# Kernel optimization log

Hardware: AMD Instinct MI355X
Metric: run time of the kernel (lower is better)

Reference implementation:

```python
import jax, jax.numpy as jnp
import numpy as np

G = 20000          # num_genes
B = 256            # batch_size
NNZ = 640000       # sparse adjacency nonzeros (avg degree 32)
K = 2              # PPR iterations
ALPHA = 0.1
NUM_CLASS = 33


def _spmm(rows, cols, vals, x):
    # y = A @ x with A sparse COO [G, G], x dense [G, B]
    return jax.ops.segment_sum(vals[:, None] * x[cols], rows, num_segments=G)


def setup_inputs() -> dict:
    key = jax.random.key(0)
    ks = jax.random.split(key, 18)
    inp = {
        "x_sample": jax.random.normal(ks[0], (B * G,), jnp.float32),
        "x_TF": jax.random.normal(ks[1], (B * G,), jnp.float32),
        "adj_rows": jax.random.randint(ks[2], (NNZ,), 0, G, jnp.int32),
        "adj_cols": jax.random.randint(ks[3], (NNZ,), 0, G, jnp.int32),
        "adj_vals": jax.random.uniform(ks[4], (NNZ,), jnp.float32) / 32.0,
        "adjT_rows": jax.random.randint(ks[5], (NNZ,), 0, G, jnp.int32),
        "adjT_cols": jax.random.randint(ks[6], (NNZ,), 0, G, jnp.int32),
        "adjT_vals": jax.random.uniform(ks[7], (NNZ,), jnp.float32) / 32.0,
        # learned scalar affine params (torch.rand(1))
        "emb_mut": jax.random.uniform(ks[8], (1,), jnp.float32),
        "bias_mut": jax.random.uniform(ks[9], (1,), jnp.float32),
        "emb_exp": jax.random.uniform(ks[10], (1,), jnp.float32),
        "bias_exp": jax.random.uniform(ks[11], (1,), jnp.float32),
        # MLP params (torch Linear layout: W [out, in])
        "W1": jax.random.normal(ks[12], (1024, G), jnp.float32) * (1.0 / np.sqrt(G)),
        "b1": jnp.zeros((1024,), jnp.float32),
        "W2": jax.random.normal(ks[13], (128, 1024), jnp.float32) * (1.0 / 32.0),
        "b2": jnp.zeros((128,), jnp.float32),
        "W3": jax.random.normal(ks[14], (NUM_CLASS, 128), jnp.float32) * (1.0 / np.sqrt(128.0)),
        "b3": jnp.zeros((NUM_CLASS,), jnp.float32),
    }
    return inp


def reference(x_sample, x_TF, adj_rows, adj_cols, adj_vals,
              adjT_rows, adjT_cols, adjT_vals,
              emb_mut, bias_mut, emb_exp, bias_exp,
              W1, b1, W2, b2, W3, b3):
    # scalar affine embedding + relu
    emb_m = jax.nn.relu(emb_mut * x_sample + bias_mut)   # [B*G]
    emb_e = jax.nn.relu(emb_exp * x_TF + bias_exp)       # [B*G]
    xs = emb_m.reshape(B, G).T                            # [G, B]
    xt = emb_e.reshape(B, G).T                            # [G, B]
    hs, ht = xs, xt
    one_m_a = 1.0 - ALPHA
    for _ in range(K):
        xs = _spmm(adj_rows, adj_cols, adj_vals, one_m_a * xs)
        xt = _spmm(adjT_rows, adjT_cols, adjT_vals, one_m_a * xt)
    xs = xs + ALPHA * hs
    xt = xt + ALPHA * ht
    hadamard = (xs * xt).T                                # [B, G]
    h1 = jax.nn.relu(hadamard @ W1.T + b1)                # [B, 1024]
    h2 = jax.nn.relu(h1 @ W2.T + b2)                      # [B, 128]
    return h2 @ W3.T + b3                                 # [B, num_class]
```

## Files before the change

### kernel.cpp

```cpp
#include <hip/hip_runtime.h>
#include <hip/hip_fp16.h>

#define G_   20000
#define B_   256
#define NNZ_ 640000
#define KCH_ 640
#define NZ_  32
#define NBUK 157
#define BCAP 4608
#define EPB  4000

typedef float f4 __attribute__((ext_vector_type(4)));
typedef _Float16 h8 __attribute__((ext_vector_type(8)));

__global__ __launch_bounds__(256) void zero_kernel(unsigned int* p, int n) {
    int i = blockIdx.x * 256 + threadIdx.x;
    if (i < n) p[i] = 0u;
}

__global__ __launch_bounds__(256) void embed_kernel(
        const float* __restrict__ xsamp, const float* __restrict__ xtf,
        const float* __restrict__ em, const float* __restrict__ bm,
        const float* __restrict__ ee, const float* __restrict__ be,
        __half* __restrict__ X0s, __half* __restrict__ X0t) {
    __shared__ float lds[64][65];
    const int t  = threadIdx.x;
    const int gb = blockIdx.x * 64, bb = blockIdx.y * 64;
    const float a_m = em[0], c_m = bm[0], a_e = ee[0], c_e = be[0];
    const int gl = t & 63, brow0 = t >> 6;
    const int cl = t & 31, row0  = t >> 5;
    const int g_l = gb + gl;
#pragma unroll
    for (int r = 0; r < 16; r++) {
        int bl = brow0 + r * 4;
        float v = 0.f;
        if (g_l < G_) v = xsamp[(size_t)(bb + bl) * G_ + g_l];
        lds[bl][gl] = fmaxf(a_m * v + c_m, 0.f);
    }
    __syncthreads();
#pragma unroll
    for (int r = 0; r < 8; r++) {
        int gl2 = row0 + r * 8;
        int g = gb + gl2;
        if (g < G_) {
            __half2 hv = __floats2half2_rn(lds[cl * 2][gl2], lds[cl * 2 + 1][gl2]);
            *(__half2*)(X0s + (size_t)g * B_ + bb + cl * 2) = hv;
        }
    }
    __syncthreads();
#pragma unroll
    for (int r = 0; r < 16; r++) {
        int bl = brow0 + r * 4;
        float v = 0.f;
        if (g_l < G_) v = xtf[(size_t)(bb + bl) * G_ + g_l];
        lds[bl][gl] = fmaxf(a_e * v + c_e, 0.f);
    }
    __syncthreads();
#pragma unroll
    for (int r = 0; r < 8; r++) {
        int gl2 = row0 + r * 8;
        int g = gb + gl2;
        if (g < G_) {
            __half2 hv = __floats2half2_rn(lds[cl * 2][gl2], lds[cl * 2 + 1][gl2]);
            *(__half2*)(X0t + (size_t)g * B_ + bb + cl * 2) = hv;
        }
    }
}

__global__ __launch_bounds__(256) void binsort_kernel(
        const int* __restrict__ rA, const int* __restrict__ cA, const float* __restrict__ vA,
        const int* __restrict__ rB, const int* __restrict__ cB, const float* __restrict__ vB,
        int2* __restrict__ metaA, int* __restrict__ cntA,
        int2* __restrict__ metaB, int* __restrict__ cntB) {
    __shared__ int2 stage[EPB];
    __shared__ unsigned char bkid[EPB];
    __shared__ int hist[NBUK], lstart[NBUK], gbase[NBUK];
    const int t = threadIdx.x;
    const int base = blockIdx.x * EPB;
    const int* rows; const int* colsp; const float* valsp; int2* meta; int* cnt;
    if (blockIdx.y == 0) { rows = rA; colsp = cA; valsp = vA; meta = metaA; cnt = cntA; }
    else                 { rows = rB; colsp = cB; valsp = vB; meta = metaB; cnt = cntB; }

    for (int i = t; i < NBUK; i += 256) hist[i] = 0;
    __syncthreads();
    for (int i = t; i < EPB; i += 256)
        atomicAdd(&hist[rows[base + i] >> 7], 1);
    __syncthreads();
    if (t == 0) {
        int s = 0;
        for (int b = 0; b < NBUK; b++) { lstart[b] = s; s += hist[b]; }
    }
    __syncthreads();
    if (t < NBUK) hist[t] = lstart[t];
    __syncthreads();
    for (int i = t; i < EPB; i += 256) {
        int r = rows[base + i];
        int c = colsp[base + i];
        float v = valsp[base + i];
        int b = r >> 7;
        int p = atomicAdd(&hist[b], 1);
        stage[p] = make_int2(((r & 127) << 24) | (c * (B_ * 2)),
                             __float_as_int(0.9f * v));
        bkid[p] = (unsigned char)b;
    }
    __syncthreads();
    if (t < NBUK) gbase[t] = atomicAdd(&cnt[t], hist[t] - lstart[t]);
    __syncthreads();
    for (int i = t; i < EPB; i += 256) {
        int b = bkid[i];
        meta[(size_t)b * BCAP + gbase[b] + (i - lstart[b])] = stage[i];
    }
}

__global__ __launch_bounds__(256) void rowsort_kernel(
        const int2* __restrict__ metaA, const int* __restrict__ cntA,
        int2* __restrict__ sortedA, int* __restrict__ rpA,
        const int2* __restrict__ metaB, const int* __restrict__ cntB,
        int2* __restrict__ sortedB, int* __restrict__ rpB) {
    __shared__ int2 stage[BCAP];
    __shared__ int2 sorted[BCAP];
    __shared__ int hist[2048];
    __shared__ int scanbuf[256];
    __shared__ int rowstart[128];
    __shared__ int carr[NBUK];
    const int t = threadIdx.x;
    const int buk = blockIdx.x;
    const int2* meta; const int* cnt; int2* outp; int* rp;
    if (blockIdx.y == 0) { meta = metaA; cnt = cntA; outp = sortedA; rp = rpA; }
    else                 { meta = metaB; cnt = cntB; outp = sortedB; rp = rpB; }

    if (t < NBUK) carr[t] = cnt[t];
    for (int i = t; i < 2048; i += 256) hist[i] = 0;
    __syncthreads();
    int bukStart = 0;
    const int nE = carr[buk];
    for (int b = 0; b < buk; b++) bukStart += carr[b];

    const int2* mp = meta + (size_t)buk * BCAP;
    for (int i = t; i < nE; i += 256) {
        int2 m = mp[i];
        stage[i] = m;
        unsigned ux = (unsigned)m.x;
        int key = ((ux >> 24) << 4) | ((ux & 0xFFFFFF) >> 20);
        atomicAdd(&hist[key], 1);
    }
    __syncthreads();
    int loc[8];
    {
        int s = 0;
#pragma unroll
        for (int i = 0; i < 8; i++) { loc[i] = s; s += hist[t * 8 + i]; }
        scanbuf[t] = s;
    }
    __syncthreads();
    for (int off = 1; off < 256; off <<= 1) {
        int v = scanbuf[t];
        int add = (t >= off) ? scanbuf[t - off] : 0;
        __syncthreads();
        scanbuf[t] = v + add;
        __syncthreads();
    }
    {
        int pre = (t == 0) ? 0 : scanbuf[t - 1];
#pragma unroll
        for (int i = 0; i < 8; i++) hist[t * 8 + i] = pre + loc[i];
    }
    __syncthreads();
    if (t < 128) rowstart[t] = hist[t << 4];
    __syncthreads();
    for (int i = t; i < nE; i += 256) {
        int2 m = stage[i];
        unsigned ux = (unsigned)m.x;
        int key = ((ux >> 24) << 4) | ((ux & 0xFFFFFF) >> 20);
        int p = atomicAdd(&hist[key], 1);
        sorted[p] = make_int2(m.x & 0xFFFFFF, m.y);
    }
    __syncthreads();
    for (int i = t; i < nE; i += 256)
        outp[bukStart + i] = sorted[i];
    if (t < 128) {
        int g = buk * 128 + t;
        if (g < G_) rp[g] = bukStart + rowstart[t];
    }
    if (buk == NBUK - 1 && t == 0) rp[G_] = bukStart + nE;
}

__global__ __launch_bounds__(256) void spmm_kernel(
        const int* __restrict__ rpA, const int2* __restrict__ metaA,
        const __half* __restrict__ xinA, __half* __restrict__ xoutA,
        const int* __restrict__ rpB, const int2* __restrict__ metaB,
        const __half* __restrict__ xinB, __half* __restrict__ xoutB) {
    const int bid   = blockIdx.x;
    const int combo = bid & 1;
    const int t = threadIdx.x;
    const int wave = t >> 6, lane = t & 63;
    const int g = (bid >> 1) * 4 + wave;
    const int* rp; const int2* meta; const __half* xin; __half* xout;
    if (combo == 0) { rp = rpA; meta = metaA; xin = xinA; xout = xoutA; }
    else            { rp = rpB; meta = metaB; xin = xinB; xout = xoutB; }
    const int beg = rp[g];
    const int n   = rp[g + 1] - beg;
    const char* xb = (const char*)xin + lane * 8;
    float a0 = 0.f, a1 = 0.f, a2 = 0.f, a3 = 0.f;
    int e = 0;
    for (; e + 4 <= n; e += 4) {
        int2 m0 = meta[beg + e],     m1 = meta[beg + e + 1];
        int2 m2 = meta[beg + e + 2], m3 = meta[beg + e + 3];
        float v0 = __int_as_float(m0.y);
        float v1 = __int_as_float(m1.y);
        float v2 = __int_as_float(m2.y);
        float v3 = __int_as_float(m3.y);
        uint2 r0 = *(const uint2*)(xb + m0.x);
        uint2 r1 = *(const uint2*)(xb + m1.x);
        uint2 r2 = *(const uint2*)(xb + m2.x);
        uint2 r3 = *(const uint2*)(xb + m3.x);
        float2 l0 = __half22float2(*(__half2*)&r0.x), h0 = __half22float2(*(__half2*)&r0.y);
        float2 l1 = __half22float2(*(__half2*)&r1.x), h1 = __half22float2(*(__half2*)&r1.y);
        float2 l2 = __half22float2(*(__half2*)&r2.x), h2 = __half22float2(*(__half2*)&r2.y);
        float2 l3 = __half22float2(*(__half2*)&r3.x), h3 = __half22float2(*(__half2*)&r3.y);
        a0 = fmaf(v0, l0.x, a0); a1 = fmaf(v0, l0.y, a1);
        a2 = fmaf(v0, h0.x, a2); a3 = fmaf(v0, h0.y, a3);
        a0 = fmaf(v1, l1.x, a0); a1 = fmaf(v1, l1.y, a1);
        a2 = fmaf(v1, h1.x, a2); a3 = fmaf(v1, h1.y, a3);
        a0 = fmaf(v2, l2.x, a0); a1 = fmaf(v2, l2.y, a1);
        a2 = fmaf(v2, h2.x, a2); a3 = fmaf(v2, h2.y, a3);
        a0 = fmaf(v3, l3.x, a0); a1 = fmaf(v3, l3.y, a1);
        a2 = fmaf(v3, h3.x, a2); a3 = fmaf(v3, h3.y, a3);
    }
    for (; e < n; ++e) {
        int2 m = meta[beg + e];
        float v = __int_as_float(m.y);
        uint2 r = *(const uint2*)(xb + m.x);
        float2 l = __half22float2(*(__half2*)&r.x), h = __half22float2(*(__half2*)&r.y);
        a0 = fmaf(v, l.x, a0); a1 = fmaf(v, l.y, a1);
        a2 = fmaf(v, h.x, a2); a3 = fmaf(v, h.y, a3);
    }
    __half2 o0 = __floats2half2_rn(a0, a1);
    __half2 o1 = __floats2half2_rn(a2, a3);
    uint2 ov;
    ov.x = *(unsigned*)&o0;
    ov.y = *(unsigned*)&o1;
    *(uint2*)((char*)xout + (size_t)g * (B_ * 2) + lane * 8) = ov;
}

__global__ __launch_bounds__(256) void combine_kernel(
        const __half* __restrict__ X2s, const __half* __restrict__ X0s,
        const __half* __restrict__ X2t, const __half* __restrict__ X0t,
        __half* __restrict__ hadBK) {
    __shared__ float lds[64][65];
    const int t = threadIdx.x;
    const int gb = blockIdx.x * 64, bb = blockIdx.y * 64;
    const int cl = t & 31, row0 = t >> 5;
#pragma unroll
    for (int r = 0; r < 8; r++) {
        int gl = row0 + r * 8;
        int g = gb + gl;
        float px = 0.f, py = 0.f;
        if (g < G_) {
            size_t idx = (size_t)g * B_ + bb + cl * 2;
            float2 x2s = __half22float2(*(const __half2*)(X2s + idx));
            float2 x0s = __half22float2(*(const __half2*)(X0s + idx));
            float2 x2t = __half22float2(*(const __half2*)(X2t + idx));
            float2 x0t = __half22float2(*(const __half2*)(X0t + idx));
            px = (x2s.x + 0.1f * x0s.x) * (x2t.x + 0.1f * x0t.x);
            py = (x2s.y + 0.1f * x0s.y) * (x2t.y + 0.1f * x0t.y);
        }
        lds[gl][cl * 2]     = px;
        lds[gl][cl * 2 + 1] = py;
    }
    __syncthreads();
#pragma unroll
    for (int r = 0; r < 8; r++) {
        int bl = row0 + r * 8;
        int g0 = gb + cl * 2;
        if (g0 < G_) {
            __half2 hv = __floats2half2_rn(lds[cl * 2][bl], lds[cl * 2 + 1][bl]);
            *(__half2*)(hadBK + (size_t)(bb + bl) * G_ + g0) = hv;
        }
    }
}

__global__ __launch_bounds__(512) void gemm1_kernel(
        const __half* __restrict__ hadBK, const float* __restrict__ W1,
        float* __restrict__ part) {
    __shared__ _Float16 a_lds[256][40];
    __shared__ _Float16 b_lds[128][40];
    const int t = threadIdx.x;
    const int lane = t & 63, wid = t >> 6;
    const int wm = wid >> 1, wn = wid & 1;
    const int l15 = lane & 15, l4 = lane >> 4;
    const int ob = blockIdx.x * 128;
    const int kb = blockIdx.y * KCH_;
    int kend = kb + KCH_; if (kend > G_) kend = G_;
    const int nsteps = (kend - kb) >> 5;
    const int ar = t >> 1, ah = t & 1;
    const int br = t >> 2, bs = t & 3;
    const _Float16* hadH = (const _Float16*)hadBK;
    const _Float16* asrc = hadH + (size_t)ar * G_ + ah * 16;
    const float*    bsrc = W1 + (size_t)(ob + br) * G_ + bs * 8;
    f4 acc[4][4] = {};
    h8 ra0 = *(const h8*)(asrc + kb);
    h8 ra1 = *(const h8*)(asrc + kb + 8);
    f4 rb0 = *(const f4*)(bsrc + kb);
    f4 rb1 = *(const f4*)(bsrc + kb + 4);
    for (int s = 0; s < nsteps; ++s) {
        *(h8*)&a_lds[ar][ah * 16]     = ra0;
        *(h8*)&a_lds[ar][ah * 16 + 8] = ra1;
        {
            h8 h;
            h[0] = (_Float16)rb0[0]; h[1] = (_Float16)rb0[1];
            h[2] = (_Float16)rb0[2]; h[3] = (_Float16)rb0[3];
            h[4] = (_Float16)rb1[0]; h[5] = (_Float16)rb1[1];
            h[6] = (_Float16)rb1[2]; h[7] = (_Float16)rb1[3];
            *(h8*)&b_lds[br][bs * 8] = h;
        }
        __syncthreads();
        if (s + 1 < nsteps) {
            const int k1 = kb + (s + 1) * 32;
            ra0 = *(const h8*)(asrc + k1);
            ra1 = *(const h8*)(asrc + k1 + 8);
            rb0 = *(const f4*)(bsrc + k1);
            rb1 = *(const f4*)(bsrc + k1 + 4);
        }
        h8 af[4], bf[4];
#pragma unroll
        for (int m = 0; m < 4; m++)
            af[m] = *(const h8*)&a_lds[wm * 64 + m * 16 + l15][l4 * 8];
#pragma unroll
        for (int n = 0; n < 4; n++)
            bf[n] = *(const h8*)&b_lds[wn * 64 + n * 16 + l15][l4 * 8];
#pragma unroll
        for (int m = 0; m < 4; m++)
#pragma unroll
            for (int n = 0; n < 4; n++)
                acc[m][n] = __builtin_amdgcn_mfma_f32_16x16x32_f16(
                    af[m], bf[n], acc[m][n], 0, 0, 0);
        __syncthreads();
    }
    const size_t zoff = (size_t)blockIdx.y * (B_ * 1024);
#pragma unroll
    for (int m = 0; m < 4; m++)
#pragma unroll
        for (int n = 0; n < 4; n++)
#pragma unroll
            for (int j = 0; j < 4; j++) {
                int b = wm * 64 + m * 16 + l4 * 4 + j;
                int o = ob + wn * 64 + n * 16 + l15;
                part[zoff + (size_t)b * 1024 + o] = acc[m][n][j];
            }
}

__global__ __launch_bounds__(256) void reduce_kernel(
        const float* __restrict__ part, const float* __restrict__ b1,
        float* __restrict__ h1) {
    int i = blockIdx.x * 256 + threadIdx.x;
    float s = 0.f;
#pragma unroll
    for (int z = 0; z < NZ_; z++) s += part[(size_t)z * 262144 + i];
    h1[i] = fmaxf(s + b1[i & 1023], 0.f);
}

__global__ __launch_bounds__(128) void gemm23_kernel(
        const float* __restrict__ h1, const float* __restrict__ W2,
        const float* __restrict__ b2, const float* __restrict__ W3,
        const float* __restrict__ b3, float* __restrict__ out) {
    __shared__ float h1row[1024];
    __shared__ float h2[128];
    const int b = blockIdx.x, t = threadIdx.x;
    *(f4*)&h1row[t * 4]       = *(const f4*)(h1 + (size_t)b * 1024 + t * 4);
    *(f4*)&h1row[512 + t * 4] = *(const f4*)(h1 + (size_t)b * 1024 + 512 + t * 4);
    __syncthreads();
    {
        float acc = b2[t];
        const f4* w  = (const f4*)(W2 + (size_t)t * 1024);
        const f4* hr = (const f4*)h1row;
        for (int k = 0; k < 256; k++) {
            f4 wv = w[k], hv = hr[k];
            acc += wv[0] * hv[0] + wv[1] * hv[1] + wv[2] * hv[2] + wv[3] * hv[3];
        }
        h2[t] = fmaxf(acc, 0.f);
    }
    __syncthreads();
    if (t < 33) {
        float acc = b3[t];
        const f4* w  = (const f4*)(W3 + (size_t)t * 128);
        const f4* hv = (const f4*)h2;
#pragma unroll
        for (int k = 0; k < 32; k++) {
            f4 a = w[k], x = hv[k];
            acc += a[0] * x[0] + a[1] * x[1] + a[2] * x[2] + a[3] * x[3];
        }
        out[b * 33 + t] = acc;
    }
}

extern "C" void kernel_launch(void* const* d_in, const int* in_sizes, int n_in,
                              void* d_out, int out_size, void* d_ws, size_t ws_size,
                              hipStream_t stream) {
    const float* x_sample  = (const float*)d_in[0];
    const float* x_TF      = (const float*)d_in[1];
    const int*   adj_rows  = (const int*)d_in[2];
    const int*   adj_cols  = (const int*)d_in[3];
    const float* adj_vals  = (const float*)d_in[4];
    const int*   adjT_rows = (const int*)d_in[5];
    const int*   adjT_cols = (const int*)d_in[6];
    const float* adjT_vals = (const float*)d_in[7];
    const float* emb_mut   = (const float*)d_in[8];
    const float* bias_mut  = (const float*)d_in[9];
    const float* emb_exp   = (const float*)d_in[10];
    const float* bias_exp  = (const float*)d_in[11];
    const float* W1 = (const float*)d_in[12];
    const float* b1 = (const float*)d_in[13];
    const float* W2 = (const float*)d_in[14];
    const float* b2 = (const float*)d_in[15];
    const float* W3 = (const float*)d_in[16];
    const float* b3 = (const float*)d_in[17];
    float* out = (float*)d_out;

    char* w = (char*)d_ws;
    auto alloc = [&](size_t bytes) {
        char* p = w; w += (bytes + 255) & ~(size_t)255; return p;
    };
    __half* X0s = (__half*)alloc(5120000 * 2);
    __half* X1s = (__half*)alloc(5120000 * 2);
    __half* X2s = (__half*)alloc(5120000 * 2);
    __half* X0t = (__half*)alloc(5120000 * 2);
    __half* X1t = (__half*)alloc(5120000 * 2);
    __half* X2t = (__half*)alloc(5120000 * 2);
    float*  part = (float*)alloc((size_t)NZ_ * 262144 * 4);
    float*  h1   = (float*)alloc(262144 * 4);
    int2*   metaA   = (int2*)alloc((size_t)NBUK * BCAP * 8);
    int2*   metaB   = (int2*)alloc((size_t)NBUK * BCAP * 8);
    int2*   sortedA = (int2*)alloc((size_t)(NNZ_ + 128) * 8);
    int2*   sortedB = (int2*)alloc((size_t)(NNZ_ + 128) * 8);
    int*    cnt   = (int*)alloc(2 * NBUK * 4);
    int*    cntA  = cnt;
    int*    cntB  = cnt + NBUK;
    int*    rpA   = (int*)alloc(20001 * 4);
    int*    rpB   = (int*)alloc(20001 * 4);
    __half* hadBK = X1s;

    zero_kernel<<<2, 256, 0, stream>>>((unsigned int*)cnt, 2 * NBUK);

    embed_kernel<<<dim3(313, 4), 256, 0, stream>>>(
        x_sample, x_TF, emb_mut, bias_mut, emb_exp, bias_exp, X0s, X0t);

    binsort_kernel<<<dim3(160, 2), 256, 0, stream>>>(
        adj_rows, adj_cols, adj_vals, adjT_rows, adjT_cols, adjT_vals,
        metaA, cntA, metaB, cntB);
    rowsort_kernel<<<dim3(NBUK, 2), 256, 0, stream>>>(
        metaA, cntA, sortedA, rpA, metaB, cntB, sortedB, rpB);

    spmm_kernel<<<10000, 256, 0, stream>>>(rpA, sortedA, X0s, X1s,
                                           rpB, sortedB, X0t, X1t);
    spmm_kernel<<<10000, 256, 0, stream>>>(rpA, sortedA, X1s, X2s,
                                           rpB, sortedB, X1t, X2t);

    combine_kernel<<<dim3(313, 4), 256, 0, stream>>>(X2s, X0s, X2t, X0t, hadBK);

    gemm1_kernel<<<dim3(8, NZ_), 512, 0, stream>>>(hadBK, W1, part);
    reduce_kernel<<<1024, 256, 0, stream>>>(part, b1, h1);
    gemm23_kernel<<<B_, 128, 0, stream>>>(h1, W2, b2, W3, b3, out);
}
```

Measured before the change: 436.3 us.

## Unroll SpMM gathers, double-buffer GEMM1 LDS, fuse split-K reduce into GEMM23

The SpMM inner loop is unrolled to 8 edges, with all index loads issued before all gathers and the row bounds made wave-uniform via readfirstlane, to raise memory-level parallelism. GEMM1 now double-buffers its LDS tiles so the next tile is written while the current one feeds MFMA, which removes one barrier per k-step. The separate split-K reduce kernel is folded into gemm23, dropping a launch and the h1 round trip through global memory. The cost is that each gemm23 block now reads its full split-K slice serially, and the larger LDS footprint may lower GEMM1 occupancy.

```diff
diff --git a/kernel.cpp b/kernel.cpp
--- a/kernel.cpp
+++ b/kernel.cpp
@@ -198,34 +198,43 @@
     const int* rp; const int2* meta; const __half* xin; __half* xout;
     if (combo == 0) { rp = rpA; meta = metaA; xin = xinA; xout = xoutA; }
     else            { rp = rpB; meta = metaB; xin = xinB; xout = xoutB; }
-    const int beg = rp[g];
-    const int n   = rp[g + 1] - beg;
+    const int beg = __builtin_amdgcn_readfirstlane(rp[g]);
+    const int n   = __builtin_amdgcn_readfirstlane(rp[g + 1]) - beg;
     const char* xb = (const char*)xin + lane * 8;
     float a0 = 0.f, a1 = 0.f, a2 = 0.f, a3 = 0.f;
     int e = 0;
-    for (; e + 4 <= n; e += 4) {
-        int2 m0 = meta[beg + e],     m1 = meta[beg + e + 1];
-        int2 m2 = meta[beg + e + 2], m3 = meta[beg + e + 3];
-        float v0 = __int_as_float(m0.y);
-        float v1 = __int_as_float(m1.y);
-        float v2 = __int_as_float(m2.y);
-        float v3 = __int_as_float(m3.y);
-        uint2 r0 = *(const uint2*)(xb + m0.x);
-        uint2 r1 = *(const uint2*)(xb + m1.x);
-        uint2 r2 = *(const uint2*)(xb + m2.x);
-        uint2 r3 = *(const uint2*)(xb + m3.x);
-        float2 l0 = __half22float2(*(__half2*)&r0.x), h0 = __half22float2(*(__half2*)&r0.y);
-        float2 l1 = __half22float2(*(__half2*)&r1.x), h1 = __half22float2(*(__half2*)&r1.y);
-        float2 l2 = __half22float2(*(__half2*)&r2.x), h2 = __half22float2(*(__half2*)&r2.y);
-        float2 l3 = __half22float2(*(__half2*)&r3.x), h3 = __half22float2(*(__half2*)&r3.y);
-        a0 = fmaf(v0, l0.x, a0); a1 = fmaf(v0, l0.y, a1);
-        a2 = fmaf(v0, h0.x, a2); a3 = fmaf(v0, h0.y, a3);
-        a0 = fmaf(v1, l1.x, a0); a1 = fmaf(v1, l1.y, a1);
-        a2 = fmaf(v1, h1.x, a2); a3 = fmaf(v1, h1.y, a3);
-        a0 = fmaf(v2, l2.x, a0); a1 = fmaf(v2, l2.y, a1);
-        a2 = fmaf(v2, h2.x, a2); a3 = fmaf(v2, h2.y, a3);
-        a0 = fmaf(v3, l3.x, a0); a1 = fmaf(v3, l3.y, a1);
-        a2 = fmaf(v3, h3.x, a2); a3 = fmaf(v3, h3.y, a3);
+    for (; e + 8 <= n; e += 8) {
+        int2 m[8];
+        uint2 r[8];
+#pragma unroll
+        for (int j = 0; j < 8; j++) m[j] = meta[beg + e + j];
+#pragma unroll
+        for (int j = 0; j < 8; j++) r[j] = *(const uint2*)(xb + m[j].x);
+#pragma unroll
+        for (int j = 0; j < 8; j++) {
+            float v = __int_as_float(m[j].y);
+            float2 l = __half22float2(*(__half2*)&r[j].x);
+            float2 h = __half22float2(*(__half2*)&r[j].y);
+            a0 = fmaf(v, l.x, a0); a1 = fmaf(v, l.y, a1);
+            a2 = fmaf(v, h.x, a2); a3 = fmaf(v, h.y, a3);
+        }
+    }
+    if (e + 4 <= n) {
+        int2 m[4];
+        uint2 r[4];
+#pragma unroll
+        for (int j = 0; j < 4; j++) m[j] = meta[beg + e + j];
+#pragma unroll
+        for (int j = 0; j < 4; j++) r[j] = *(const uint2*)(xb + m[j].x);
+#pragma unroll
+        for (int j = 0; j < 4; j++) {
+            float v = __int_as_float(m[j].y);
+            float2 l = __half22float2(*(__half2*)&r[j].x);
+            float2 h = __half22float2(*(__half2*)&r[j].y);
+            a0 = fmaf(v, l.x, a0); a1 = fmaf(v, l.y, a1);
+            a2 = fmaf(v, h.x, a2); a3 = fmaf(v, h.y, a3);
+        }
+        e += 4;
     }
     for (; e < n; ++e) {
         int2 m = meta[beg + e];
@@ -283,8 +292,8 @@
 __global__ __launch_bounds__(512) void gemm1_kernel(
         const __half* __restrict__ hadBK, const float* __restrict__ W1,
         float* __restrict__ part) {
-    __shared__ _Float16 a_lds[256][40];
-    __shared__ _Float16 b_lds[128][40];
+    __shared__ _Float16 a_lds[2][256][40];
+    __shared__ _Float16 b_lds[2][128][40];
     const int t = threadIdx.x;
     const int lane = t & 63, wid = t >> 6;
     const int wm = wid >> 1, wn = wid & 1;
@@ -303,18 +312,19 @@
     h8 ra1 = *(const h8*)(asrc + kb + 8);
     f4 rb0 = *(const f4*)(bsrc + kb);
     f4 rb1 = *(const f4*)(bsrc + kb + 4);
+    *(h8*)&a_lds[0][ar][ah * 16]     = ra0;
+    *(h8*)&a_lds[0][ar][ah * 16 + 8] = ra1;
+    {
+        h8 h;
+        h[0] = (_Float16)rb0[0]; h[1] = (_Float16)rb0[1];
+        h[2] = (_Float16)rb0[2]; h[3] = (_Float16)rb0[3];
+        h[4] = (_Float16)rb1[0]; h[5] = (_Float16)rb1[1];
+        h[6] = (_Float16)rb1[2]; h[7] = (_Float16)rb1[3];
+        *(h8*)&b_lds[0][br][bs * 8] = h;
+    }
+    __syncthreads();
+    int p = 0;
     for (int s = 0; s < nsteps; ++s) {
-        *(h8*)&a_lds[ar][ah * 16]     = ra0;
-        *(h8*)&a_lds[ar][ah * 16 + 8] = ra1;
-        {
-            h8 h;
-            h[0] = (_Float16)rb0[0]; h[1] = (_Float16)rb0[1];
-            h[2] = (_Float16)rb0[2]; h[3] = (_Float16)rb0[3];
-            h[4] = (_Float16)rb1[0]; h[5] = (_Float16)rb1[1];
-            h[6] = (_Float16)rb1[2]; h[7] = (_Float16)rb1[3];
-            *(h8*)&b_lds[br][bs * 8] = h;
-        }
-        __syncthreads();
         if (s + 1 < nsteps) {
             const int k1 = kb + (s + 1) * 32;
             ra0 = *(const h8*)(asrc + k1);
@@ -325,17 +335,28 @@
         h8 af[4], bf[4];
 #pragma unroll
         for (int m = 0; m < 4; m++)
-            af[m] = *(const h8*)&a_lds[wm * 64 + m * 16 + l15][l4 * 8];
+            af[m] = *(const h8*)&a_lds[p][wm * 64 + m * 16 + l15][l4 * 8];
 #pragma unroll
         for (int n = 0; n < 4; n++)
-            bf[n] = *(const h8*)&b_lds[wn * 64 + n * 16 + l15][l4 * 8];
+            bf[n] = *(const h8*)&b_lds[p][wn * 64 + n * 16 + l15][l4 * 8];
 #pragma unroll
         for (int m = 0; m < 4; m++)
 #pragma unroll
             for (int n = 0; n < 4; n++)
                 acc[m][n] = __builtin_amdgcn_mfma_f32_16x16x32_f16(
                     af[m], bf[n], acc[m][n], 0, 0, 0);
-        __syncthreads();
+        if (s + 1 < nsteps) {
+            *(h8*)&a_lds[p ^ 1][ar][ah * 16]     = ra0;
+            *(h8*)&a_lds[p ^ 1][ar][ah * 16 + 8] = ra1;
+            h8 h;
+            h[0] = (_Float16)rb0[0]; h[1] = (_Float16)rb0[1];
+            h[2] = (_Float16)rb0[2]; h[3] = (_Float16)rb0[3];
+            h[4] = (_Float16)rb1[0]; h[5] = (_Float16)rb1[1];
+            h[6] = (_Float16)rb1[2]; h[7] = (_Float16)rb1[3];
+            *(h8*)&b_lds[p ^ 1][br][bs * 8] = h;
+            __syncthreads();
+            p ^= 1;
+        }
     }
     const size_t zoff = (size_t)blockIdx.y * (B_ * 1024);
 #pragma unroll
@@ -350,25 +371,26 @@
             }
 }
 
-__global__ __launch_bounds__(256) void reduce_kernel(
+__global__ __launch_bounds__(128) void gemm23_kernel(
         const float* __restrict__ part, const float* __restrict__ b1,
-        float* __restrict__ h1) {
-    int i = blockIdx.x * 256 + threadIdx.x;
-    float s = 0.f;
-#pragma unroll
-    for (int z = 0; z < NZ_; z++) s += part[(size_t)z * 262144 + i];
-    h1[i] = fmaxf(s + b1[i & 1023], 0.f);
-}
-
-__global__ __launch_bounds__(128) void gemm23_kernel(
-        const float* __restrict__ h1, const float* __restrict__ W2,
-        const float* __restrict__ b2, const float* __restrict__ W3,
-        const float* __restrict__ b3, float* __restrict__ out) {
+        const float* __restrict__ W2, const float* __restrict__ b2,
+        const float* __restrict__ W3, const float* __restrict__ b3,
+        float* __restrict__ out) {
     __shared__ float h1row[1024];
     __shared__ float h2[128];
     const int b = blockIdx.x, t = threadIdx.x;
-    *(f4*)&h1row[t * 4]       = *(const f4*)(h1 + (size_t)b * 1024 + t * 4);
-    *(f4*)&h1row[512 + t * 4] = *(const f4*)(h1 + (size_t)b * 1024 + 512 + t * 4);
+#pragma unroll
+    for (int seg = 0; seg < 2; seg++) {
+        int o4 = t + seg * 128;
+        f4 s = {0.f, 0.f, 0.f, 0.f};
+        for (int z = 0; z < NZ_; z++)
+            s += ((const f4*)(part + (size_t)z * 262144 + (size_t)b * 1024))[o4];
+        s += ((const f4*)b1)[o4];
+        f4 r;
+        r[0] = fmaxf(s[0], 0.f); r[1] = fmaxf(s[1], 0.f);
+        r[2] = fmaxf(s[2], 0.f); r[3] = fmaxf(s[3], 0.f);
+        ((f4*)h1row)[o4] = r;
+    }
     __syncthreads();
     {
         float acc = b2[t];
@@ -428,7 +450,6 @@
     __half* X1t = (__half*)alloc(5120000 * 2);
     __half* X2t = (__half*)alloc(5120000 * 2);
     float*  part = (float*)alloc((size_t)NZ_ * 262144 * 4);
-    float*  h1   = (float*)alloc(262144 * 4);
     int2*   metaA   = (int2*)alloc((size_t)NBUK * BCAP * 8);
     int2*   metaB   = (int2*)alloc((size_t)NBUK * BCAP * 8);
     int2*   sortedA = (int2*)alloc((size_t)(NNZ_ + 128) * 8);
@@ -459,6 +480,5 @@
     combine_kernel<<<dim3(313, 4), 256, 0, stream>>>(X2s, X0s, X2t, X0t, hadBK);
 
     gemm1_kernel<<<dim3(8, NZ_), 512, 0, stream>>>(hadBK, W1, part);
-    reduce_kernel<<<1024, 256, 0, stream>>>(part, b1, h1);
-    gemm23_kernel<<<B_, 128, 0, stream>>>(h1, W2, b2, W3, b3, out);
-}
+    gemm23_kernel<<<B_, 128, 0, stream>>>(part, b1, W2, b2, W3, b3, out);
+}
```

New measurement: 432.9 us. No clear change (-0.8%).
